# Kernel tuning notes

Hardware: AMD Instinct MI355X
Metric: run time of the kernel (lower is better)

## Reference

```python
import jax, jax.numpy as jnp
from jax import lax
import numpy as np

B, C, H, W, K = 4, 64, 64, 64, 3
PAD = K // 2
EPS = 1e-5


def _conv2d(x, w, b, pad):
    y = lax.conv_general_dilated(x, w, (1, 1), [(pad, pad), (pad, pad)],
                                 dimension_numbers=('NCHW', 'OIHW', 'NCHW'))
    return y + b[None, :, None, None]


def setup_inputs() -> dict:
    key = jax.random.key(0)
    ks = jax.random.split(key, 13)
    n = lambda k, shape, s: jax.random.normal(k, shape, jnp.float32) * s
    return {
        'x':     jax.random.normal(ks[0], (B, C, H, W), jnp.float32),
        'w1':    n(ks[1], (4 * C, C, K, K), 0.04),      # Conv2d(C, 4C, 3, pad=1)
        'b1':    n(ks[2], (4 * C,), 0.01),
        'w2':    n(ks[3], (16 * C, 4 * C, K, K), 0.02), # Conv2d(4C, 16C, 3, pad=1)
        'b2':    n(ks[4], (16 * C,), 0.01),
        'w3':    n(ks[5], (C, 16 * C), 0.02),           # Conv2d(16C, C, 1)
        'b3':    n(ks[6], (C,), 0.01),
        'wd':    n(ks[7], (C * K * K, C), 0.05),        # Conv2d(C, C*k*k, 1) on 1x1 map
        'bd':    n(ks[8], (C * K * K,), 0.01),
        'w4':    n(ks[9], (C, B), 0.1),                 # Conv2d(B, C, 1)  (broadcast-bug channel dim = B)
        'b4':    n(ks[10], (C,), 0.01),
        'gamma': jax.random.uniform(ks[11], (C,), jnp.float32, 0.5, 1.5),
        'beta':  n(ks[12], (C,), 0.05),
    }


def reference(x, w1, b1, w2, b2, w3, b3, wd, bd, w4, b4, gamma, beta):
    # stacked convs + relu
    h = jax.nn.relu(_conv2d(x, w1, b1, 1))                 # (B, 4C, H, W)
    h = jax.nn.relu(_conv2d(h, w2, b2, 1))                 # (B, 16C, H, W)
    h = jnp.einsum('bchw,oc->bohw', h, w3) + b3[None, :, None, None]  # (B, C, H, W)

    # dynamic per-sample kernel weights from global average pool
    pooled = h.mean((2, 3))                                # (B, C)
    dw = (pooled @ wd.T + bd).reshape(B, C, K * K)         # (B, C, k*k)

    # F.unfold(h, k, padding=k//2) -> (B, C, k*k, H, W), torch channel-major, taps row-major
    hp = jnp.pad(h, ((0, 0), (0, 0), (PAD, PAD), (PAD, PAD)))
    patches = jnp.stack([hp[:, :, i:i + H, j:j + W]
                         for i in range(K) for j in range(K)], axis=2)  # (B, C, 9, H, W)

    # faithful to torch broadcast: (B,1,C,9,H,W) * (1,B,C,9,1,1), sum(dim=3) twice -> (B,B,C,W)
    xd = jnp.einsum('acphw,bcp->abcw', patches, dw)        # sums over taps p and H

    # Conv2d(in=B, out=C, 1x1) over the second axis (channel dim = B due to the bug)
    out = jnp.einsum('abcw,ob->aocw', xd, w4) + b4[None, :, None, None]  # (B, C, C, W)

    # BatchNorm2d(C), training mode: batch statistics over dims (0, 2, 3)
    mean = out.mean((0, 2, 3), keepdims=True)
    var = ((out - mean) ** 2).mean((0, 2, 3), keepdims=True)
    out = (out - mean) * lax.rsqrt(var + EPS)
    return out * gamma[None, :, None, None] + beta[None, :, None, None]
```

## Files before the change

### kernel.cpp

```cpp
#include <hip/hip_runtime.h>
#include <hip/hip_bf16.h>
#include <math.h>

typedef unsigned short ushort;
typedef __attribute__((ext_vector_type(8))) short bf16x8;
typedef __attribute__((ext_vector_type(4))) float f32x4;
typedef __attribute__((ext_vector_type(8))) ushort ushort8;

__device__ inline ushort f2bf(float f) {
  __hip_bfloat16 h = __float2bfloat16(f);
  return *reinterpret_cast<ushort*>(&h);
}

typedef __attribute__((address_space(3))) unsigned int lds_u32;
typedef __attribute__((address_space(1))) const unsigned int glb_u32;
__device__ __forceinline__ void gl2lds16(const ushort* g, ushort* l) {
  __builtin_amdgcn_global_load_lds((glb_u32*)g, (lds_u32*)l, 16, 0, 0);
}

#define S_BARRIER asm volatile("s_barrier" ::: "memory")
#define WAITV0 asm volatile("s_waitcnt vmcnt(0)" ::: "memory")

__global__ __launch_bounds__(256) void pack_all(
    const float* __restrict__ x, const float* __restrict__ w1,
    const float* __restrict__ w2, ushort* __restrict__ xn_pad,
    ushort* __restrict__ w1p, ushort* __restrict__ w2p,
    ushort* __restrict__ h1n_pad, float* __restrict__ zbase) {
  int blk = blockIdx.x;
  int tid = threadIdx.x;
  __shared__ float ld[64][65];
  if (blk < 264) {
    int b = blk / 66, yp = blk % 66;
    if (yp == 0 || yp == 65) {
      for (int i = tid; i < 66 * 64; i += 256) {
        int xp = i >> 6, c = i & 63;
        xn_pad[((size_t)(b * 66 + xp)) * 4224 + yp * 64 + c] = 0;
      }
      return;
    }
    int y = yp - 1;
    int xx = tid & 63;
#pragma unroll
    for (int i = 0; i < 16; ++i) {
      int c = i * 4 + (tid >> 6);
      ld[c][xx] = x[((b * 64 + c) * 64 + y) * 64 + xx];
    }
    __syncthreads();
    for (int i = tid; i < 2 * 64; i += 256) {
      int side = i >> 6, c = i & 63;
      xn_pad[((size_t)(b * 66 + (side ? 65 : 0))) * 4224 + yp * 64 + c] = 0;
    }
    for (int u = tid; u < 64 * 8; u += 256) {
      int xp = u >> 3, cg = u & 7;
      ushort8 v;
#pragma unroll
      for (int j = 0; j < 8; ++j) v[j] = f2bf(ld[cg * 8 + j][xp]);
      *reinterpret_cast<ushort8*>(
          &xn_pad[((size_t)(b * 66 + xp + 1)) * 4224 + yp * 64 + cg * 8]) = v;
    }
  } else if (blk < 328) {
    int idx = (blk - 264) * 256 + tid;
    float v[9];
#pragma unroll
    for (int t = 0; t < 9; ++t) v[t] = w1[idx * 9 + t];
    int oc = idx >> 6, c = idx & 63;
#pragma unroll
    for (int tp = 0; tp < 9; ++tp)
      w1p[(tp * 256 + oc) * 64 + c] = f2bf(v[(tp % 3) * 3 + tp / 3]);
  } else if (blk < 1352) {
    int idx = (blk - 328) * 256 + tid;
    float v[9];
#pragma unroll
    for (int t = 0; t < 9; ++t) v[t] = w2[(size_t)idx * 9 + t];
    int oc = idx >> 8, c = idx & 255;
#pragma unroll
    for (int tp = 0; tp < 9; ++tp)
      w2p[((size_t)tp * 1024 + oc) * 256 + c] = f2bf(v[(tp % 3) * 3 + tp / 3]);
  } else if (blk < 2392) {
    int k = blk - 1352;
    int b = k / 260, p = k % 260;
    int yp, xp;
    if (p < 66) { yp = 0; xp = p; }
    else if (p < 132) { yp = 65; xp = p - 66; }
    else if (p < 196) { yp = p - 132 + 1; xp = 0; }
    else { yp = p - 196 + 1; xp = 65; }
    h1n_pad[((size_t)(b * 66 + xp) * 66 + yp) * 256 + tid] = 0;
  } else {
    if (tid < 96) {
      float4 z = {0.f, 0.f, 0.f, 0.f};
      *reinterpret_cast<float4*>(zbase + tid * 4) = z;
    }
  }
}

template<int C1B, int NOC, int MODE>
__global__ __launch_bounds__(256, 2) void conv_gemm3(
    const ushort* __restrict__ in_pad, const ushort* __restrict__ wpack,
    const float* __restrict__ bias, ushort* __restrict__ outp,
    float* __restrict__ U, float* __restrict__ h0raw,
    float* __restrict__ h63raw) {
  constexpr int CIN = C1B * 64;
  constexpr int NSTEP = C1B * 9;
  constexpr int BN = 128;
  constexpr int BUFU = BN * 64;
  constexpr int ACH = 4 * 66 * 8;
  extern __shared__ ushort lds[];
  ushort* Araw = lds;
  ushort* Bb = lds + ACH * 8;
  int tid = threadIdx.x;
  int wid = tid >> 6, lane = tid & 63;
  int lrow = lane & 15, lk = lane >> 4;
  int wm = wid >> 1, wn = wid & 1;
  int bx = blockIdx.x, by = blockIdx.y;
  if constexpr (MODE == 1) {
    int id = bx + 128 * by;
    int swz = (id & 7) * 128 + (id >> 3);
    bx = swz & 127;
    by = swz >> 7;
  }
  int P0 = bx * 128;
  int b = P0 >> 12;
  int x0 = (P0 & 4095) >> 6;
  int ocB = by * BN;
  f32x4 acc[4][4] = {};

  int aoff[9];
#pragma unroll
  for (int it = 0; it < 9; ++it) {
    int ch = it * 256 + tid;
    int slot = ch >> 3, cg = ch & 7;
    int xs = slot % 66;
    int cgp = cg ^ (xs & 7);
    aoff[it] = slot * CIN + cgp * 8;
  }
  int boff[4];
#pragma unroll
  for (int it = 0; it < 4; ++it) {
    int ch = it * 256 + tid;
    int oc = ch >> 3, cg = ch & 7;
    int cgp = cg ^ (oc & 7);
    boff[it] = oc * CIN + cgp * 8;
  }

  auto stageA = [&](int cb) {
    const ushort* asrc = in_pad + (size_t)(b * 66 + x0) * 66 * CIN + cb * 64;
#pragma unroll
    for (int it = 0; it < 9; ++it) {
      int basech = it * 256 + wid * 64;
      if (basech < ACH)
        gl2lds16(asrc + aoff[it], Araw + basech * 8);
    }
  };
  auto stageB = [&](int sstep, int q) {
    const ushort* wsrc =
        wpack + ((size_t)(sstep % 9) * NOC + ocB) * CIN + (sstep / 9) * 64;
    ushort* dbase = Bb + q * BUFU;
#pragma unroll
    for (int it = 0; it < 4; ++it)
      gl2lds16(wsrc + boff[it], dbase + (it * 256 + wid * 64) * 8);
  };

  stageA(0);
  stageB(0, 0);
  WAITV0;
  S_BARRIER;

#pragma unroll 1
  for (int cb = 0; cb < C1B; ++cb) {
#pragma unroll 1
    for (int t = 0; t < 9; ++t) {
      int step = cb * 9 + t;
      int ky = t / 3, kx = t - ky * 3;
      const ushort* bcur = Bb + (step & 1) * BUFU;
      bool pre = (step + 1 < NSTEP);
      if (pre) stageB(step + 1, (step + 1) & 1);
#pragma unroll
      for (int ks = 0; ks < 2; ++ks) {
        bf16x8 af[4], bfv[4];
#pragma unroll
        for (int mf = 0; mf < 4; ++mf) {
          int Y = mf * 16 + lrow;
          int xs = Y + kx;
          int slot = (wm + ky) * 66 + xs;
          int ko = ((ks * 64 + lk * 16) ^ ((xs & 7) << 4)) >> 1;
          af[mf] = *reinterpret_cast<const bf16x8*>(Araw + slot * 64 + ko);
        }
#pragma unroll
        for (int nf = 0; nf < 4; ++nf) {
          int oc_l = wn * 64 + nf * 16 + lrow;
          int ko = ((ks * 64 + lk * 16) ^ ((oc_l & 7) << 4)) >> 1;
          bfv[nf] = *reinterpret_cast<const bf16x8*>(bcur + oc_l * 64 + ko);
        }
        __builtin_amdgcn_s_setprio(1);
#pragma unroll
        for (int mf = 0; mf < 4; ++mf)
#pragma unroll
          for (int nf = 0; nf < 4; ++nf)
            acc[mf][nf] = __builtin_amdgcn_mfma_f32_16x16x32_bf16(
                af[mf], bfv[nf], acc[mf][nf], 0, 0, 0);
        __builtin_amdgcn_s_setprio(0);
      }
      if (t == 8 && cb + 1 < C1B) {
        S_BARRIER;
        stageA(cb + 1);
        WAITV0;
        S_BARRIER;
      } else {
        WAITV0;
        S_BARRIER;
      }
    }
  }

  if constexpr (MODE == 0) {
#pragma unroll
    for (int nf = 0; nf < 4; ++nf) {
      int oc = ocB + wn * 64 + nf * 16 + lrow;
      float bv = bias[oc];
#pragma unroll
      for (int mf = 0; mf < 4; ++mf) {
        int m0 = wm * 64 + mf * 16 + lk * 4;
#pragma unroll
        for (int r = 0; r < 4; ++r) {
          float vv = fmaxf(acc[mf][nf][r] + bv, 0.f);
          int px = P0 + m0 + r;
          int bb = px >> 12, X = (px >> 6) & 63, Y = px & 63;
          outp[((size_t)(bb * 66 + X + 1) * 66 + Y + 1) * NOC + oc] = f2bf(vv);
        }
      }
    }
  } else {
    int X = x0 + wm;
#pragma unroll
    for (int nf = 0; nf < 4; ++nf) {
      int oc = ocB + wn * 64 + nf * 16 + lrow;
      float bv = bias[oc];
      float s = 0.f;
#pragma unroll
      for (int mf = 0; mf < 4; ++mf) {
#pragma unroll
        for (int r = 0; r < 4; ++r) {
          float vv = fmaxf(acc[mf][nf][r] + bv, 0.f);
          s += vv;
          int Y = mf * 16 + lk * 4 + r;
          if (Y == 0)
            h0raw[((size_t)(b * 64 + X)) * 1024 + oc] = vv;
          else if (Y == 63)
            h63raw[((size_t)(b * 64 + X)) * 1024 + oc] = vv;
        }
      }
      s += __shfl_xor(s, 16);
      s += __shfl_xor(s, 32);
      if (lk == 0)
        U[((size_t)(b * 64 + X)) * 1024 + oc] = s;
    }
  }
}

__global__ __launch_bounds__(256) void tailB(
    const float* __restrict__ U, const float* __restrict__ h0raw,
    const float* __restrict__ h63raw, const float* __restrict__ w3,
    const float* __restrict__ b3, float* __restrict__ T,
    float* __restrict__ h0, float* __restrict__ h63,
    float* __restrict__ pooled) {
  int blk = blockIdx.x;
  int a = blk >> 6, xx = blk & 63;
  __shared__ float Ul[1024], R0[1024], R63[1024];
  int tid = threadIdx.x;
  const float* ub = U + (size_t)blk * 1024;
  const float* r0b = h0raw + (size_t)blk * 1024;
  const float* r6b = h63raw + (size_t)blk * 1024;
  *reinterpret_cast<float4*>(&Ul[tid * 4]) =
      *reinterpret_cast<const float4*>(&ub[tid * 4]);
  *reinterpret_cast<float4*>(&R0[tid * 4]) =
      *reinterpret_cast<const float4*>(&r0b[tid * 4]);
  *reinterpret_cast<float4*>(&R63[tid * 4]) =
      *reinterpret_cast<const float4*>(&r6b[tid * 4]);
  __syncthreads();
  int c = tid >> 2, g = tid & 3;
  const float* w3r = w3 + c * 1024 + g * 256;
  float sT = 0.f, s0 = 0.f, s6 = 0.f;
  for (int k = 0; k < 256; k += 4) {
    float4 w = *reinterpret_cast<const float4*>(w3r + k);
    int kk = g * 256 + k;
    float4 uu = *reinterpret_cast<const float4*>(&Ul[kk]);
    float4 a0 = *reinterpret_cast<const float4*>(&R0[kk]);
    float4 a6 = *reinterpret_cast<const float4*>(&R63[kk]);
    sT = fmaf(uu.x, w.x, sT); sT = fmaf(uu.y, w.y, sT);
    sT = fmaf(uu.z, w.z, sT); sT = fmaf(uu.w, w.w, sT);
    s0 = fmaf(a0.x, w.x, s0); s0 = fmaf(a0.y, w.y, s0);
    s0 = fmaf(a0.z, w.z, s0); s0 = fmaf(a0.w, w.w, s0);
    s6 = fmaf(a6.x, w.x, s6); s6 = fmaf(a6.y, w.y, s6);
    s6 = fmaf(a6.z, w.z, s6); s6 = fmaf(a6.w, w.w, s6);
  }
  sT += __shfl_xor(sT, 1); sT += __shfl_xor(sT, 2);
  s0 += __shfl_xor(s0, 1); s0 += __shfl_xor(s0, 2);
  s6 += __shfl_xor(s6, 1); s6 += __shfl_xor(s6, 2);
  if (g == 0) {
    float bv = b3[c];
    float tf = sT + 64.f * bv;
    T[(a * 64 + c) * 64 + xx] = tf;
    h0[(a * 64 + c) * 64 + xx] = s0 + bv;
    h63[(a * 64 + c) * 64 + xx] = s6 + bv;
    atomicAdd(&pooled[a * 64 + c], tf * (1.f / 4096.f));
  }
}

__global__ __launch_bounds__(256) void xdout(
    const float* __restrict__ T, const float* __restrict__ h0,
    const float* __restrict__ h63, const float* __restrict__ pooled,
    const float* __restrict__ wd, const float* __restrict__ bd,
    const float* __restrict__ w4, const float* __restrict__ b4,
    float* __restrict__ out, float* __restrict__ stats) {
  int a = blockIdx.x >> 4, cg = blockIdx.x & 15;
  int t = threadIdx.x;
  __shared__ float dwl[4][4][9];
  __shared__ float redS[256], redQ[256];
  if (t < 144) {
    int bb = t / 36, rem = t % 36, cj = rem / 9, p = rem % 9;
    int r = (cg * 4 + cj) * 9 + p;
    float s = bd[r];
    const float* pr = pooled + bb * 64;
    const float* wr = wd + r * 64;
    for (int cc = 0; cc < 64; ++cc) s = fmaf(pr[cc], wr[cc], s);
    dwl[bb][cj][p] = s;
  }
  __syncthreads();
  int c4 = t >> 6, xx = t & 63;
  int lane = t & 63, wv = t >> 6;
  int c = cg * 4 + c4;
  const float* Tp = T + (a * 64 + c) * 64;
  const float* H0 = h0 + (a * 64 + c) * 64;
  const float* H63 = h63 + (a * 64 + c) * 64;
  float xd4[4] = {0.f, 0.f, 0.f, 0.f};
#pragma unroll
  for (int j = 0; j < 3; ++j) {
    int xi = xx + j - 1;
    if (xi >= 0 && xi < 64) {
      float tv = Tp[xi];
      float S0 = tv - H63[xi];
      float S2 = tv - H0[xi];
#pragma unroll
      for (int bb = 0; bb < 4; ++bb) {
        xd4[bb] = fmaf(dwl[bb][c4][j], S0, xd4[bb]);
        xd4[bb] = fmaf(dwl[bb][c4][3 + j], tv, xd4[bb]);
        xd4[bb] = fmaf(dwl[bb][c4][6 + j], S2, xd4[bb]);
      }
    }
  }
  float* op = out + (size_t)a * 262144 + c * 64 + xx;
  for (int o = 0; o < 64; ++o) {
    float v = b4[o];
#pragma unroll
    for (int bb = 0; bb < 4; ++bb) v = fmaf(w4[o * 4 + bb], xd4[bb], v);
    op[o * 4096] = v;
    float sv = v, sq = v * v;
#pragma unroll
    for (int off = 32; off > 0; off >>= 1) {
      sv += __shfl_down(sv, off);
      sq += __shfl_down(sq, off);
    }
    if (lane == 0) { redS[wv * 64 + o] = sv; redQ[wv * 64 + o] = sq; }
  }
  __syncthreads();
  if (t < 64) {
    float S = redS[t] + redS[64 + t] + redS[128 + t] + redS[192 + t];
    float Q = redQ[t] + redQ[64 + t] + redQ[128 + t] + redQ[192 + t];
    atomicAdd(&stats[t], S);
    atomicAdd(&stats[64 + t], Q);
  }
}

__global__ __launch_bounds__(256) void bnapply_kernel(
    float* __restrict__ out, const float* __restrict__ stats,
    const float* __restrict__ gamma, const float* __restrict__ beta) {
  int idx = blockIdx.x * 256 + threadIdx.x;
  int o = (idx >> 12) & 63;
  float mean = stats[o] * (1.f / 16384.f);
  float var = stats[64 + o] * (1.f / 16384.f) - mean * mean;
  float rstd = rsqrtf(var + 1e-5f);
  out[idx] = (out[idx] - mean) * rstd * gamma[o] + beta[o];
}

extern "C" void kernel_launch(void* const* d_in, const int* in_sizes, int n_in,
                              void* d_out, int out_size, void* d_ws,
                              size_t ws_size, hipStream_t stream) {
  const float* x     = (const float*)d_in[0];
  const float* w1    = (const float*)d_in[1];
  const float* b1    = (const float*)d_in[2];
  const float* w2    = (const float*)d_in[3];
  const float* b2    = (const float*)d_in[4];
  const float* w3    = (const float*)d_in[5];
  const float* b3    = (const float*)d_in[6];
  const float* wd    = (const float*)d_in[7];
  const float* bd    = (const float*)d_in[8];
  const float* w4    = (const float*)d_in[9];
  const float* b4    = (const float*)d_in[10];
  const float* gamma = (const float*)d_in[11];
  const float* beta  = (const float*)d_in[12];
  float* out = (float*)d_out;

  ushort* us = (ushort*)d_ws;
  ushort* h1n_pad = us;
  ushort* xn_pad  = us + 4460544;
  ushort* w1p     = us + 5575680;
  ushort* w2p     = us + 5723136;
  float* fbase    = (float*)(us + 8082432);
  float* Ub      = fbase;
  float* pooled  = Ub + 262144;
  float* stats   = pooled + 256;
  float* Tb      = stats + 128;
  float* h0b     = Tb + 16384;
  float* h63b    = h0b + 16384;
  float* h0raw   = h63b + 16384;
  float* h63raw  = h0raw + 262144;

  pack_all<<<2393, 256, 0, stream>>>(x, w1, w2, xn_pad, w1p, w2p, h1n_pad,
                                     pooled);

  hipFuncSetAttribute(
      reinterpret_cast<const void*>(conv_gemm3<1, 256, 0>),
      hipFuncAttributeMaxDynamicSharedMemorySize, 66560);
  hipFuncSetAttribute(
      reinterpret_cast<const void*>(conv_gemm3<4, 1024, 1>),
      hipFuncAttributeMaxDynamicSharedMemorySize, 66560);

  conv_gemm3<1, 256, 0>
      <<<dim3(128, 2), 256, 66560, stream>>>(xn_pad, w1p, b1, h1n_pad,
                                             nullptr, nullptr, nullptr);
  conv_gemm3<4, 1024, 1>
      <<<dim3(128, 8), 256, 66560, stream>>>(h1n_pad, w2p, b2, nullptr,
                                             Ub, h0raw, h63raw);

  tailB<<<256, 256, 0, stream>>>(Ub, h0raw, h63raw, w3, b3, Tb, h0b, h63b,
                                 pooled);
  xdout<<<64, 256, 0, stream>>>(Tb, h0b, h63b, pooled, wd, bd, w4, b4, out,
                                stats);
  bnapply_kernel<<<4096, 256, 0, stream>>>(out, stats, gamma, beta);
}
```

Baseline: 129.1 us.

## Switch conv GEMM from 16x16x32 to 32x32x16 bf16 MFMA tiles

```diff
diff --git a/kernel.cpp b/kernel.cpp
--- a/kernel.cpp
+++ b/kernel.cpp
@@ -4,7 +4,7 @@
 
 typedef unsigned short ushort;
 typedef __attribute__((ext_vector_type(8))) short bf16x8;
-typedef __attribute__((ext_vector_type(4))) float f32x4;
+typedef __attribute__((ext_vector_type(16))) float f32x16;
 typedef __attribute__((ext_vector_type(8))) ushort ushort8;
 
 __device__ inline ushort f2bf(float f) {
@@ -109,7 +109,7 @@
   ushort* Bb = lds + ACH * 8;
   int tid = threadIdx.x;
   int wid = tid >> 6, lane = tid & 63;
-  int lrow = lane & 15, lk = lane >> 4;
+  int l31 = lane & 31, hi = lane >> 5;
   int wm = wid >> 1, wn = wid & 1;
   int bx = blockIdx.x, by = blockIdx.y;
   if constexpr (MODE == 1) {
@@ -122,7 +122,7 @@
   int b = P0 >> 12;
   int x0 = (P0 & 4095) >> 6;
   int ocB = by * BN;
-  f32x4 acc[4][4] = {};
+  f32x16 acc[2][2] = {};
 
   int aoff[9];
 #pragma unroll
@@ -175,29 +175,36 @@
       bool pre = (step + 1 < NSTEP);
       if (pre) stageB(step + 1, (step + 1) & 1);
 #pragma unroll
-      for (int ks = 0; ks < 2; ++ks) {
-        bf16x8 af[4], bfv[4];
-#pragma unroll
-        for (int mf = 0; mf < 4; ++mf) {
-          int Y = mf * 16 + lrow;
-          int xs = Y + kx;
-          int slot = (wm + ky) * 66 + xs;
-          int ko = ((ks * 64 + lk * 16) ^ ((xs & 7) << 4)) >> 1;
-          af[mf] = *reinterpret_cast<const bf16x8*>(Araw + slot * 64 + ko);
-        }
-#pragma unroll
-        for (int nf = 0; nf < 4; ++nf) {
-          int oc_l = wn * 64 + nf * 16 + lrow;
-          int ko = ((ks * 64 + lk * 16) ^ ((oc_l & 7) << 4)) >> 1;
-          bfv[nf] = *reinterpret_cast<const bf16x8*>(bcur + oc_l * 64 + ko);
+      for (int kp = 0; kp < 2; ++kp) {
+        bf16x8 af[2][2], bfv[2][2];
+#pragma unroll
+        for (int kq = 0; kq < 2; ++kq) {
+          int gr = (kp * 2 + kq) * 2 + hi;
+#pragma unroll
+          for (int mt = 0; mt < 2; ++mt) {
+            int xs = mt * 32 + l31 + kx;
+            int slot = (wm + ky) * 66 + xs;
+            int ko = (gr ^ (xs & 7)) * 8;
+            af[kq][mt] =
+                *reinterpret_cast<const bf16x8*>(Araw + slot * 64 + ko);
+          }
+#pragma unroll
+          for (int nt = 0; nt < 2; ++nt) {
+            int oc_l = wn * 64 + nt * 32 + l31;
+            int ko = (gr ^ (oc_l & 7)) * 8;
+            bfv[kq][nt] =
+                *reinterpret_cast<const bf16x8*>(bcur + oc_l * 64 + ko);
+          }
         }
         __builtin_amdgcn_s_setprio(1);
 #pragma unroll
-        for (int mf = 0; mf < 4; ++mf)
-#pragma unroll
-          for (int nf = 0; nf < 4; ++nf)
-            acc[mf][nf] = __builtin_amdgcn_mfma_f32_16x16x32_bf16(
-                af[mf], bfv[nf], acc[mf][nf], 0, 0, 0);
+        for (int kq = 0; kq < 2; ++kq)
+#pragma unroll
+          for (int mt = 0; mt < 2; ++mt)
+#pragma unroll
+            for (int nt = 0; nt < 2; ++nt)
+              acc[mt][nt] = __builtin_amdgcn_mfma_f32_32x32x16_bf16(
+                  af[kq][mt], bfv[kq][nt], acc[mt][nt], 0, 0, 0);
         __builtin_amdgcn_s_setprio(0);
       }
       if (t == 8 && cb + 1 < C1B) {
@@ -212,47 +219,47 @@
     }
   }
 
+  int X = x0 + wm;
   if constexpr (MODE == 0) {
 #pragma unroll
-    for (int nf = 0; nf < 4; ++nf) {
-      int oc = ocB + wn * 64 + nf * 16 + lrow;
+    for (int nt = 0; nt < 2; ++nt) {
+      int oc = ocB + wn * 64 + nt * 32 + l31;
       float bv = bias[oc];
 #pragma unroll
-      for (int mf = 0; mf < 4; ++mf) {
-        int m0 = wm * 64 + mf * 16 + lk * 4;
-#pragma unroll
-        for (int r = 0; r < 4; ++r) {
-          float vv = fmaxf(acc[mf][nf][r] + bv, 0.f);
-          int px = P0 + m0 + r;
-          int bb = px >> 12, X = (px >> 6) & 63, Y = px & 63;
-          outp[((size_t)(bb * 66 + X + 1) * 66 + Y + 1) * NOC + oc] = f2bf(vv);
+      for (int mt = 0; mt < 2; ++mt) {
+#pragma unroll
+        for (int reg = 0; reg < 16; ++reg) {
+          int Y = mt * 32 + (reg & 3) + 8 * (reg >> 2) + 4 * hi;
+          float vv = fmaxf(acc[mt][nt][reg] + bv, 0.f);
+          outp[((size_t)(b * 66 + X + 1) * 66 + Y + 1) * NOC + oc] = f2bf(vv);
         }
       }
     }
   } else {
-    int X = x0 + wm;
-#pragma unroll
-    for (int nf = 0; nf < 4; ++nf) {
-      int oc = ocB + wn * 64 + nf * 16 + lrow;
+#pragma unroll
+    for (int nt = 0; nt < 2; ++nt) {
+      int oc = ocB + wn * 64 + nt * 32 + l31;
       float bv = bias[oc];
       float s = 0.f;
-#pragma unroll
-      for (int mf = 0; mf < 4; ++mf) {
-#pragma unroll
-        for (int r = 0; r < 4; ++r) {
-          float vv = fmaxf(acc[mf][nf][r] + bv, 0.f);
+      float v0 = 0.f, v63 = 0.f;
+#pragma unroll
+      for (int mt = 0; mt < 2; ++mt) {
+#pragma unroll
+        for (int reg = 0; reg < 16; ++reg) {
+          float vv = fmaxf(acc[mt][nt][reg] + bv, 0.f);
           s += vv;
-          int Y = mf * 16 + lk * 4 + r;
-          if (Y == 0)
-            h0raw[((size_t)(b * 64 + X)) * 1024 + oc] = vv;
-          else if (Y == 63)
-            h63raw[((size_t)(b * 64 + X)) * 1024 + oc] = vv;
+          if (mt == 0 && reg == 0) v0 = vv;
+          if (mt == 1 && reg == 15) v63 = vv;
         }
       }
-      s += __shfl_xor(s, 16);
       s += __shfl_xor(s, 32);
-      if (lk == 0)
-        U[((size_t)(b * 64 + X)) * 1024 + oc] = s;
+      size_t ui = ((size_t)(b * 64 + X)) * 1024 + oc;
+      if (hi == 0) {
+        U[ui] = s;
+        h0raw[ui] = v0;
+      } else {
+        h63raw[ui] = v63;
+      }
     }
   }
 }
```

Result: slower. 136.1 us (+5.4%).

## Fuse tail kernels into one cooperative kernel with grid-wide syncs

Applied to the files above, without the earlier changes.

```diff
diff --git a/kernel.cpp b/kernel.cpp
--- a/kernel.cpp
+++ b/kernel.cpp
@@ -1,6 +1,9 @@
 #include <hip/hip_runtime.h>
 #include <hip/hip_bf16.h>
+#include <hip/hip_cooperative_groups.h>
 #include <math.h>
+
+namespace cg = cooperative_groups;
 
 typedef unsigned short ushort;
 typedef __attribute__((ext_vector_type(8))) short bf16x8;
@@ -257,68 +260,70 @@
   }
 }
 
-__global__ __launch_bounds__(256) void tailB(
+__global__ __launch_bounds__(256) void tail_fused(
     const float* __restrict__ U, const float* __restrict__ h0raw,
     const float* __restrict__ h63raw, const float* __restrict__ w3,
-    const float* __restrict__ b3, float* __restrict__ T,
+    const float* __restrict__ b3, const float* __restrict__ wd,
+    const float* __restrict__ bd, const float* __restrict__ w4,
+    const float* __restrict__ b4, const float* __restrict__ gamma,
+    const float* __restrict__ beta, float* __restrict__ T,
     float* __restrict__ h0, float* __restrict__ h63,
-    float* __restrict__ pooled) {
+    float* __restrict__ pooled, float* __restrict__ stats,
+    float* __restrict__ out) {
+  cg::grid_group grid = cg::this_grid();
   int blk = blockIdx.x;
-  int a = blk >> 6, xx = blk & 63;
+  int tid = threadIdx.x;
   __shared__ float Ul[1024], R0[1024], R63[1024];
-  int tid = threadIdx.x;
-  const float* ub = U + (size_t)blk * 1024;
-  const float* r0b = h0raw + (size_t)blk * 1024;
-  const float* r6b = h63raw + (size_t)blk * 1024;
-  *reinterpret_cast<float4*>(&Ul[tid * 4]) =
-      *reinterpret_cast<const float4*>(&ub[tid * 4]);
-  *reinterpret_cast<float4*>(&R0[tid * 4]) =
-      *reinterpret_cast<const float4*>(&r0b[tid * 4]);
-  *reinterpret_cast<float4*>(&R63[tid * 4]) =
-      *reinterpret_cast<const float4*>(&r6b[tid * 4]);
-  __syncthreads();
-  int c = tid >> 2, g = tid & 3;
-  const float* w3r = w3 + c * 1024 + g * 256;
-  float sT = 0.f, s0 = 0.f, s6 = 0.f;
-  for (int k = 0; k < 256; k += 4) {
-    float4 w = *reinterpret_cast<const float4*>(w3r + k);
-    int kk = g * 256 + k;
-    float4 uu = *reinterpret_cast<const float4*>(&Ul[kk]);
-    float4 a0 = *reinterpret_cast<const float4*>(&R0[kk]);
-    float4 a6 = *reinterpret_cast<const float4*>(&R63[kk]);
-    sT = fmaf(uu.x, w.x, sT); sT = fmaf(uu.y, w.y, sT);
-    sT = fmaf(uu.z, w.z, sT); sT = fmaf(uu.w, w.w, sT);
-    s0 = fmaf(a0.x, w.x, s0); s0 = fmaf(a0.y, w.y, s0);
-    s0 = fmaf(a0.z, w.z, s0); s0 = fmaf(a0.w, w.w, s0);
-    s6 = fmaf(a6.x, w.x, s6); s6 = fmaf(a6.y, w.y, s6);
-    s6 = fmaf(a6.z, w.z, s6); s6 = fmaf(a6.w, w.w, s6);
-  }
-  sT += __shfl_xor(sT, 1); sT += __shfl_xor(sT, 2);
-  s0 += __shfl_xor(s0, 1); s0 += __shfl_xor(s0, 2);
-  s6 += __shfl_xor(s6, 1); s6 += __shfl_xor(s6, 2);
-  if (g == 0) {
-    float bv = b3[c];
-    float tf = sT + 64.f * bv;
-    T[(a * 64 + c) * 64 + xx] = tf;
-    h0[(a * 64 + c) * 64 + xx] = s0 + bv;
-    h63[(a * 64 + c) * 64 + xx] = s6 + bv;
-    atomicAdd(&pooled[a * 64 + c], tf * (1.f / 4096.f));
-  }
-}
-
-__global__ __launch_bounds__(256) void xdout(
-    const float* __restrict__ T, const float* __restrict__ h0,
-    const float* __restrict__ h63, const float* __restrict__ pooled,
-    const float* __restrict__ wd, const float* __restrict__ bd,
-    const float* __restrict__ w4, const float* __restrict__ b4,
-    float* __restrict__ out, float* __restrict__ stats) {
-  int a = blockIdx.x >> 4, cg = blockIdx.x & 15;
-  int t = threadIdx.x;
   __shared__ float dwl[4][4][9];
-  __shared__ float redS[256], redQ[256];
-  if (t < 144) {
-    int bb = t / 36, rem = t % 36, cj = rem / 9, p = rem % 9;
-    int r = (cg * 4 + cj) * 9 + p;
+  __shared__ float redS[4][16], redQ[4][16];
+  __shared__ float mrs[2][64];
+
+  {
+    int a = blk >> 6, xx = blk & 63;
+    const float* ub = U + (size_t)blk * 1024;
+    const float* r0b = h0raw + (size_t)blk * 1024;
+    const float* r6b = h63raw + (size_t)blk * 1024;
+    *reinterpret_cast<float4*>(&Ul[tid * 4]) =
+        *reinterpret_cast<const float4*>(&ub[tid * 4]);
+    *reinterpret_cast<float4*>(&R0[tid * 4]) =
+        *reinterpret_cast<const float4*>(&r0b[tid * 4]);
+    *reinterpret_cast<float4*>(&R63[tid * 4]) =
+        *reinterpret_cast<const float4*>(&r6b[tid * 4]);
+    __syncthreads();
+    int c = tid >> 2, g = tid & 3;
+    const float* w3r = w3 + c * 1024 + g * 256;
+    float sT = 0.f, s0 = 0.f, s6 = 0.f;
+    for (int k = 0; k < 256; k += 4) {
+      float4 w = *reinterpret_cast<const float4*>(w3r + k);
+      int kk = g * 256 + k;
+      float4 uu = *reinterpret_cast<const float4*>(&Ul[kk]);
+      float4 a0 = *reinterpret_cast<const float4*>(&R0[kk]);
+      float4 a6 = *reinterpret_cast<const float4*>(&R63[kk]);
+      sT = fmaf(uu.x, w.x, sT); sT = fmaf(uu.y, w.y, sT);
+      sT = fmaf(uu.z, w.z, sT); sT = fmaf(uu.w, w.w, sT);
+      s0 = fmaf(a0.x, w.x, s0); s0 = fmaf(a0.y, w.y, s0);
+      s0 = fmaf(a0.z, w.z, s0); s0 = fmaf(a0.w, w.w, s0);
+      s6 = fmaf(a6.x, w.x, s6); s6 = fmaf(a6.y, w.y, s6);
+      s6 = fmaf(a6.z, w.z, s6); s6 = fmaf(a6.w, w.w, s6);
+    }
+    sT += __shfl_xor(sT, 1); sT += __shfl_xor(sT, 2);
+    s0 += __shfl_xor(s0, 1); s0 += __shfl_xor(s0, 2);
+    s6 += __shfl_xor(s6, 1); s6 += __shfl_xor(s6, 2);
+    if (g == 0) {
+      float bv = b3[c];
+      float tf = sT + 64.f * bv;
+      T[(a * 64 + c) * 64 + xx] = tf;
+      h0[(a * 64 + c) * 64 + xx] = s0 + bv;
+      h63[(a * 64 + c) * 64 + xx] = s6 + bv;
+      atomicAdd(&pooled[a * 64 + c], tf * (1.f / 4096.f));
+    }
+  }
+  grid.sync();
+
+  int a = blk >> 6, cgi = (blk >> 2) & 15, og = blk & 3;
+  if (tid < 144) {
+    int bb = tid / 36, rem = tid % 36, cj = rem / 9, p = rem % 9;
+    int r = (cgi * 4 + cj) * 9 + p;
     float s = bd[r];
     const float* pr = pooled + bb * 64;
     const float* wr = wd + r * 64;
@@ -326,9 +331,9 @@
     dwl[bb][cj][p] = s;
   }
   __syncthreads();
-  int c4 = t >> 6, xx = t & 63;
-  int lane = t & 63, wv = t >> 6;
-  int c = cg * 4 + c4;
+  int c4 = tid >> 6, xx = tid & 63;
+  int lane = tid & 63, wv = tid >> 6;
+  int c = cgi * 4 + c4;
   const float* Tp = T + (a * 64 + c) * 64;
   const float* H0 = h0 + (a * 64 + c) * 64;
   const float* H63 = h63 + (a * 64 + c) * 64;
@@ -348,38 +353,45 @@
       }
     }
   }
-  float* op = out + (size_t)a * 262144 + c * 64 + xx;
-  for (int o = 0; o < 64; ++o) {
+  float vout[16];
+#pragma unroll
+  for (int oi = 0; oi < 16; ++oi) {
+    int o = og * 16 + oi;
     float v = b4[o];
 #pragma unroll
     for (int bb = 0; bb < 4; ++bb) v = fmaf(w4[o * 4 + bb], xd4[bb], v);
-    op[o * 4096] = v;
+    vout[oi] = v;
     float sv = v, sq = v * v;
 #pragma unroll
     for (int off = 32; off > 0; off >>= 1) {
       sv += __shfl_down(sv, off);
       sq += __shfl_down(sq, off);
     }
-    if (lane == 0) { redS[wv * 64 + o] = sv; redQ[wv * 64 + o] = sq; }
+    if (lane == 0) { redS[wv][oi] = sv; redQ[wv][oi] = sq; }
   }
   __syncthreads();
-  if (t < 64) {
-    float S = redS[t] + redS[64 + t] + redS[128 + t] + redS[192 + t];
-    float Q = redQ[t] + redQ[64 + t] + redQ[128 + t] + redQ[192 + t];
-    atomicAdd(&stats[t], S);
-    atomicAdd(&stats[64 + t], Q);
-  }
-}
-
-__global__ __launch_bounds__(256) void bnapply_kernel(
-    float* __restrict__ out, const float* __restrict__ stats,
-    const float* __restrict__ gamma, const float* __restrict__ beta) {
-  int idx = blockIdx.x * 256 + threadIdx.x;
-  int o = (idx >> 12) & 63;
-  float mean = stats[o] * (1.f / 16384.f);
-  float var = stats[64 + o] * (1.f / 16384.f) - mean * mean;
-  float rstd = rsqrtf(var + 1e-5f);
-  out[idx] = (out[idx] - mean) * rstd * gamma[o] + beta[o];
+  if (tid < 16) {
+    float S = redS[0][tid] + redS[1][tid] + redS[2][tid] + redS[3][tid];
+    float Q = redQ[0][tid] + redQ[1][tid] + redQ[2][tid] + redQ[3][tid];
+    atomicAdd(&stats[og * 16 + tid], S);
+    atomicAdd(&stats[64 + og * 16 + tid], Q);
+  }
+  grid.sync();
+
+  if (tid < 64) {
+    float mean = stats[tid] * (1.f / 16384.f);
+    float var = stats[64 + tid] * (1.f / 16384.f) - mean * mean;
+    mrs[0][tid] = mean;
+    mrs[1][tid] = rsqrtf(var + 1e-5f);
+  }
+  __syncthreads();
+  float* op = out + (size_t)a * 262144 + c * 64 + xx;
+#pragma unroll
+  for (int oi = 0; oi < 16; ++oi) {
+    int o = og * 16 + oi;
+    op[(size_t)o * 4096] =
+        (vout[oi] - mrs[0][o]) * mrs[1][o] * gamma[o] + beta[o];
+  }
 }
 
 extern "C" void kernel_launch(void* const* d_in, const int* in_sizes, int n_in,
@@ -432,9 +444,11 @@
       <<<dim3(128, 8), 256, 66560, stream>>>(h1n_pad, w2p, b2, nullptr,
                                              Ub, h0raw, h63raw);
 
-  tailB<<<256, 256, 0, stream>>>(Ub, h0raw, h63raw, w3, b3, Tb, h0b, h63b,
-                                 pooled);
-  xdout<<<64, 256, 0, stream>>>(Tb, h0b, h63b, pooled, wd, bd, w4, b4, out,
-                                stats);
-  bnapply_kernel<<<4096, 256, 0, stream>>>(out, stats, gamma, beta);
-}
+  void* targs[] = {(void*)&Ub,    (void*)&h0raw, (void*)&h63raw, (void*)&w3,
+                   (void*)&b3,    (void*)&wd,    (void*)&bd,     (void*)&w4,
+                   (void*)&b4,    (void*)&gamma, (void*)&beta,   (void*)&Tb,
+                   (void*)&h0b,   (void*)&h63b,  (void*)&pooled,
+                   (void*)&stats, (void*)&out};
+  hipLaunchCooperativeKernel(reinterpret_cast<const void*>(tail_fused),
+                             dim3(256), dim3(256), targs, 0, stream);
+}
```

Result: slower. 169.8 us (+31.6%).
